# Optimization experiments

Hardware: AMD Instinct MI355X
Metric: run time of the kernel (lower is better)

The kernel has to match this reference:

```python
import jax, jax.numpy as jnp
import numpy as np

N, C, T, V = 16, 256, 400, 27
S, CI, O = 2, 64, 256      # num_subset, inter_channels, out_channels
OFFSET = 2                  # LearnedPositionalEmbedding offset
EPS = 1e-5                  # BatchNorm eps (inference/eval mode)


def _bn(x, g, b, m, v):
    # BatchNorm2d in eval mode: (x - mean)/sqrt(var+eps)*gamma + beta, per-channel
    return (x - m[None, :, None, None]) / jnp.sqrt(v[None, :, None, None] + EPS) \
        * g[None, :, None, None] + b[None, :, None, None]


def setup_inputs() -> dict:
    key = jax.random.key(0)
    ks = jax.random.split(key, 24)
    u = lambda k, s: jax.random.uniform(k, s, jnp.float32, 0.5, 1.5)
    r = lambda k, s, sc: jax.random.normal(k, s, jnp.float32) * sc
    d = {}
    d['x'] = jax.random.normal(ks[0], (N, C, T, V), jnp.float32)
    # learned positional embedding table: (num_frame + offset, num_node)
    d['pe'] = r(ks[1], (400 + OFFSET, V), 0.02)
    # in_nets: 1x1 conv C -> 2*S*CI
    d['in_w'] = r(ks[2], (2 * S * CI, C), 0.02)
    d['in_b'] = jnp.zeros((2 * S * CI,), jnp.float32)
    d['alphas'] = jnp.ones((1, S, 1, 1), jnp.float32)
    d['att0'] = jnp.ones((1, S, V, V), jnp.float32) / V   # attention0s
    # out_nets: 1x1 conv S*C -> O, then BN1
    d['out_w'] = r(ks[3], (O, S * C), 0.02)
    d['out_b'] = jnp.zeros((O,), jnp.float32)
    d['bn1_g'] = u(ks[4], (O,)); d['bn1_b'] = r(ks[5], (O,), 0.1)
    d['bn1_m'] = r(ks[6], (O,), 0.1); d['bn1_v'] = u(ks[7], (O,))
    # ff_nets: 1x1 conv O -> O, then BN2
    d['ff_w'] = r(ks[8], (O, O), 0.02)
    d['ff_b'] = jnp.zeros((O,), jnp.float32)
    d['bn2_g'] = u(ks[9], (O,)); d['bn2_b'] = r(ks[10], (O,), 0.1)
    d['bn2_m'] = r(ks[11], (O,), 0.1); d['bn2_v'] = u(ks[12], (O,))
    # out_nett: (3,1) temporal conv O -> O, then BN3
    d['t_w'] = r(ks[13], (O, O, 3, 1), 0.02)
    d['t_b'] = jnp.zeros((O,), jnp.float32)
    d['bn3_g'] = u(ks[14], (O,)); d['bn3_b'] = r(ks[15], (O,), 0.1)
    d['bn3_m'] = r(ks[16], (O,), 0.1); d['bn3_v'] = u(ks[17], (O,))
    return d


def reference(x, pe, in_w, in_b, alphas, att0, out_w, out_b,
              bn1_g, bn1_b, bn1_m, bn1_v, ff_w, ff_b,
              bn2_g, bn2_b, bn2_m, bn2_v, t_w, t_b,
              bn3_g, bn3_b, bn3_m, bn3_v):
    n, c, t, v = x.shape
    # learned positional embedding over frame index (shared across batch*channel)
    pos = pe[jnp.arange(t) + OFFSET]              # (T, V)
    y = x + pos[None, None, :, :]                 # (N, C, T, V)
    # in_nets 1x1 conv -> q, k
    qk = jnp.einsum('nctv,oc->notv', y, in_w) + in_b[None, :, None, None]
    qk = qk.reshape(n, 2 * S, CI, t, v)
    q, k = qk[:, :S], qk[:, S:]                   # (N, S, CI, T, V) each
    attn = jnp.einsum('nsctu,nsctv->nsuv', q, k) / (CI * t) * alphas + att0
    attn = jax.nn.softmax(attn, axis=-1)          # (N, S, V, V)  (dropout p=0)
    # re-aggregate values with original x
    y2 = jnp.einsum('nctu,nsuv->nsctv', x, attn).reshape(n, S * c, t, v)
    y2 = jnp.einsum('nctv,oc->notv', y2, out_w) + out_b[None, :, None, None]
    y2 = _bn(y2, bn1_g, bn1_b, bn1_m, bn1_v)
    y1 = jax.nn.leaky_relu(x + y2, 0.1)           # downs1 = identity (C==O)
    y2 = jnp.einsum('nctv,oc->notv', y1, ff_w) + ff_b[None, :, None, None]
    y2 = _bn(y2, bn2_g, bn2_b, bn2_m, bn2_v)
    y1 = jax.nn.leaky_relu(x + y2, 0.1)           # downs2 = identity
    # temporal branch (use_temporal_att=False): (3,1) conv + BN + residual
    z = jax.lax.conv_general_dilated(
        y1, t_w, window_strides=(1, 1), padding=((1, 1), (0, 0)),
        dimension_numbers=('NCHW', 'OIHW', 'NCHW')) + t_b[None, :, None, None]
    z = _bn(z, bn3_g, bn3_b, bn3_m, bn3_v)
    return jax.nn.leaky_relu(y1 + z, 0.1)         # downt2 = identity
```

## Files before the change

### kernel.cpp

```cpp
#include <hip/hip_runtime.h>
#include <hip/hip_bf16.h>
#include <cstddef>

#define NBATCH 16
#define CCH    256
#define TT     400
#define VV     27
#define TV     10800
#define EPSV   1e-5f
#define P2     10854

typedef __attribute__((ext_vector_type(8))) short  short8;
typedef __attribute__((ext_vector_type(4))) float  floatx4;

__device__ __forceinline__ unsigned short f2bu(float f) {
    __hip_bfloat16 h = __float2bfloat16(f);
    return *(unsigned short*)&h;
}
__device__ __forceinline__ float bu2f(unsigned short u) {
    union { float f; unsigned int i; } c; c.i = ((unsigned int)u) << 16; return c.f;
}
__device__ __forceinline__ void gl_lds16(const void* g, void* l) {
    __builtin_amdgcn_global_load_lds(
        (const __attribute__((address_space(1))) void*)g,
        (__attribute__((address_space(3))) void*)l, 16, 0, 0);
}

template<int KC, int MODE>
__global__ __launch_bounds__(512) void mfma_gemm(
    const unsigned short* __restrict__ X8,
    const unsigned short* __restrict__ W8,
    const float* __restrict__ bias,
    const float* __restrict__ bng, const float* __restrict__ bnb,
    const float* __restrict__ bnm, const float* __restrict__ bnv,
    const unsigned short* __restrict__ res8,
    const float* __restrict__ pe,
    float* __restrict__ outf,
    unsigned short* __restrict__ out8)
{
    constexpr int XPITCH = (MODE == 3) ? P2 : TV;
    constexpr int XOFF   = (MODE == 3) ? 27 : 0;
    constexpr int XROWS  = (MODE == 3) ? 32 : (KC / 8);
    constexpr int OPITCH = (MODE == 2) ? P2 : TV;
    constexpr int OOFF   = (MODE == 2) ? 27 : 0;
    constexpr int NSTEP  = KC / 32;

    __shared__ short Ws[3][4096];
    __shared__ short Xs[3][8192];
    __shared__ float scs[128], shs[128];

    const int tid  = threadIdx.x;
    const int wid  = tid >> 6;
    const int lane = tid & 63;
    const int quad = lane >> 4, col = lane & 15;

    const int bid = blockIdx.x;
    const int g   = bid >> 4;
    const int r   = bid & 15;
    const int oy  = r >> 3;
    const int j   = g * 8 + (r & 7);
    const int px  = j % 43;
    const int n   = j / 43;
    const int p0 = px * 256;
    const int o0 = oy * 128;

    const int wo = (wid >> 2) * 64;
    const int wp = (wid & 3) * 64;

    const size_t nX = (size_t)n * XROWS * XPITCH;

    auto stage = [&](int buf, int step) {
        int k0, c0, pshift = 0;
        if constexpr (MODE == 3) {
            const int ccs = step / 3;
            const int kt  = step - ccs * 3;
            k0 = kt * 256 + ccs * 32;
            c0 = ccs * 32;
            pshift = 27 * (kt - 1);
        } else {
            k0 = step * 32;
            c0 = k0;
        }
        #pragma unroll
        for (int q = 0; q < 3; q++) {
            const int ci = wid * 3 + q;
            if (ci < 8) {
                const int kg = ci >> 1, half = ci & 1;
                const size_t woff = ((size_t)((k0 >> 3) + kg) * 256 + o0 + half * 64 + lane) * 8;
                gl_lds16(W8 + woff, &Ws[buf][ci * 512]);
            } else {
                const int xi = ci - 8;
                const int kg = xi >> 2, q4 = xi & 3;
                const size_t xoff = (nX + (size_t)((c0 >> 3) + kg) * XPITCH
                                     + XOFF + p0 + pshift + q4 * 64 + lane) * 8;
                gl_lds16(X8 + xoff, &Xs[buf][xi * 512]);
            }
        }
    };

    floatx4 acc[4][4];
    #pragma unroll
    for (int i = 0; i < 4; i++)
        #pragma unroll
        for (int j2 = 0; j2 < 4; j2++)
            acc[i][j2] = (floatx4){0.f, 0.f, 0.f, 0.f};

    stage(0, 0);
    stage(1, 1);

    int cur = 0;
    for (int step = 0; step < NSTEP; ++step) {
        if (step + 1 < NSTEP) asm volatile("s_waitcnt vmcnt(3)" ::: "memory");
        else                  asm volatile("s_waitcnt vmcnt(0)" ::: "memory");
        __builtin_amdgcn_s_barrier();
        if (step + 2 < NSTEP) stage((cur + 2 >= 3) ? cur - 1 : cur + 2, step + 2);
        short8 a[4], b[4];
        #pragma unroll
        for (int i = 0; i < 4; i++)
            a[i] = *(const short8*)&Ws[cur][quad * 1024 + (wo + i * 16 + col) * 8];
        #pragma unroll
        for (int j2 = 0; j2 < 4; j2++)
            b[j2] = *(const short8*)&Xs[cur][quad * 2048 + (wp + j2 * 16 + col) * 8];
        __builtin_amdgcn_s_setprio(1);
        #pragma unroll
        for (int i = 0; i < 4; i++)
            #pragma unroll
            for (int j2 = 0; j2 < 4; j2++)
                acc[i][j2] = __builtin_amdgcn_mfma_f32_16x16x32_bf16(a[i], b[j2], acc[i][j2], 0, 0, 0);
        __builtin_amdgcn_s_setprio(0);
        cur = (cur == 2) ? 0 : cur + 1;
    }

    __syncthreads();

    if (tid < 128) {
        const int o = o0 + tid;
        float sc, sh;
        if constexpr (MODE == 0) { sc = 1.f; sh = bias[o]; }
        else {
            const float g2 = bng[o], b2 = bnb[o], m = bnm[o], v2 = bnv[o];
            sc = g2 * rsqrtf(v2 + EPSV);
            sh = bias[o] * sc + b2 - m * sc;
        }
        scs[tid] = sc; shs[tid] = sh;
    }
    __syncthreads();

    #pragma unroll
    for (int i = 0; i < 4; i++) {
        const int ol = wo + i * 16 + quad * 4;
        const int ob = o0 + ol;
        #pragma unroll
        for (int j2 = 0; j2 < 4; j2++) {
            const int p = p0 + wp + j2 * 16 + col;
            if (p >= TV) continue;
            float v[4];
            #pragma unroll
            for (int r2 = 0; r2 < 4; r2++)
                v[r2] = acc[i][j2][r2] * scs[ol + r2] + shs[ol + r2];
            if constexpr (MODE == 3) {
                const size_t roff = ((size_t)n * 32 * P2 + (size_t)(ob >> 3) * P2 + 27 + p) * 8 + (ob & 7);
                union { unsigned long long u64; unsigned short us[4]; } rr;
                rr.u64 = *(const unsigned long long*)&res8[roff];
                #pragma unroll
                for (int r2 = 0; r2 < 4; r2++) {
                    float t = v[r2] + bu2f(rr.us[r2]);
                    t = t > 0.f ? t : 0.1f * t;
                    outf[((size_t)n * 256 + ob + r2) * TV + p] = t;
                }
            } else if constexpr (MODE == 0) {
                union { unsigned long long u64; unsigned short us[4]; } pk;
                #pragma unroll
                for (int r2 = 0; r2 < 4; r2++) pk.us[r2] = f2bu(v[r2]);
                *(unsigned long long*)&out8[((size_t)n * 32 * TV
                    + (size_t)(ob >> 3) * TV + p) * 8 + (ob & 7)] = pk.u64;
            } else {
                const float pev = pe[p + 54];
                const size_t roff = ((size_t)n * 32 * TV + (size_t)(ob >> 3) * TV + p) * 8 + (ob & 7);
                union { unsigned long long u64; unsigned short us[4]; } rr;
                rr.u64 = *(const unsigned long long*)&res8[roff];
                union { unsigned long long u64; unsigned short us[4]; } pk;
                #pragma unroll
                for (int r2 = 0; r2 < 4; r2++) {
                    float t = v[r2] + (bu2f(rr.us[r2]) - pev);
                    t = t > 0.f ? t : 0.1f * t;
                    pk.us[r2] = f2bu(t);
                }
                *(unsigned long long*)&out8[((size_t)n * 32 * OPITCH
                    + (size_t)(ob >> 3) * OPITCH + OOFF + p) * 8 + (ob & 7)] = pk.u64;
            }
        }
    }
}

__global__ __launch_bounds__(256) void prep_xpe(
    const float* __restrict__ x, const float* __restrict__ pe,
    unsigned short* __restrict__ xpe8)
{
    const int p = blockIdx.x * 256 + threadIdx.x;
    const int cg = blockIdx.y, n = blockIdx.z;
    if (p >= TV) return;
    const float pev = pe[p + 54];
    const float* xp = x + ((size_t)n * 256 + cg * 8) * TV + p;
    union { unsigned short us[8]; uint4 q; } pk;
    #pragma unroll
    for (int r = 0; r < 8; r++)
        pk.us[r] = f2bu(xp[(size_t)r * TV] + pev);
    *(uint4*)&xpe8[(((size_t)n * 32 + cg) * TV + p) * 8] = pk.q;
}

__global__ void pack_w(const float* __restrict__ w, unsigned short* __restrict__ w8,
                       int KCc, int conv)
{
    const int idx = blockIdx.x * 256 + threadIdx.x;
    if (idx >= 256 * KCc) return;
    const int o = idx / KCc, k = idx - o * KCc;
    float v;
    if (conv) { const int c = k & 255, kt = k >> 8; v = w[((size_t)o * 256 + c) * 3 + kt]; }
    else v = w[(size_t)o * KCc + k];
    w8[((size_t)(k >> 3) * 256 + o) * 8 + (k & 7)] = f2bu(v);
}

__global__ void zero_pads(unsigned short* __restrict__ y1b8) {
    unsigned short* base = y1b8 + (size_t)blockIdx.x * P2 * 8;
    for (int i = threadIdx.x; i < 27 * 8; i += 256) {
        base[i] = 0;
        base[10827 * 8 + i] = 0;
    }
}

__global__ __launch_bounds__(256) void attn_logits_mfma(
    const unsigned short* __restrict__ qk8, float* __restrict__ logits)
{
    __shared__ float red[4][32][33];
    const int tid  = threadIdx.x;
    const int wid  = tid >> 6;
    const int lane = tid & 63;
    const int quad = lane >> 4, col = lane & 15;
    const int tch = blockIdx.x;
    const int ns  = blockIdx.y;
    const int n = ns >> 1, s = ns & 1;
    const int t0 = tch * 16 + wid * 4;

    const unsigned short* qb = qk8 + (size_t)(n * 32 + s * 8) * TV * 8;
    const unsigned short* kb = qk8 + (size_t)(n * 32 + 16 + s * 8) * TV * 8;

    floatx4 acc[2][2];
    #pragma unroll
    for (int i = 0; i < 2; i++)
        #pragma unroll
        for (int j = 0; j < 2; j++)
            acc[i][j] = (floatx4){0.f, 0.f, 0.f, 0.f};

    #pragma unroll
    for (int ti = 0; ti < 4; ti++) {
        const int t = t0 + ti;
        #pragma unroll
        for (int kk = 0; kk < 2; kk++) {
            const size_t ro = ((size_t)(kk * 4 + quad) * TV + t * 27 + col) * 8;
            const short8 a0 = *(const short8*)&qb[ro];
            const short8 a1 = *(const short8*)&qb[ro + 128];
            const short8 b0 = *(const short8*)&kb[ro];
            const short8 b1 = *(const short8*)&kb[ro + 128];
            acc[0][0] = __builtin_amdgcn_mfma_f32_16x16x32_bf16(a0, b0, acc[0][0], 0, 0, 0);
            acc[0][1] = __builtin_amdgcn_mfma_f32_16x16x32_bf16(a0, b1, acc[0][1], 0, 0, 0);
            acc[1][0] = __builtin_amdgcn_mfma_f32_16x16x32_bf16(a1, b0, acc[1][0], 0, 0, 0);
            acc[1][1] = __builtin_amdgcn_mfma_f32_16x16x32_bf16(a1, b1, acc[1][1], 0, 0, 0);
        }
    }

    #pragma unroll
    for (int i = 0; i < 2; i++)
        #pragma unroll
        for (int j = 0; j < 2; j++)
            #pragma unroll
            for (int r = 0; r < 4; r++)
                red[wid][i * 16 + quad * 4 + r][j * 16 + col] = acc[i][j][r];
    __syncthreads();
    for (int e = tid; e < 729; e += 256) {
        const int u = e / 27, v = e - u * 27;
        atomicAdd(&logits[(size_t)ns * 729 + e],
                  red[0][u][v] + red[1][u][v] + red[2][u][v] + red[3][u][v]);
    }
}

__global__ __launch_bounds__(64) void attn_softmax(
    const float* __restrict__ logits, const float* __restrict__ alphas,
    const float* __restrict__ att0, float* __restrict__ attn)
{
    const int ns = blockIdx.x;
    const int s = ns & 1;
    const int u = threadIdx.x;
    if (u < 27) {
        float row[27];
        const float alpha = alphas[s];
        const float inv_ct = 1.f / 25600.f;
        float m = -1e30f;
        for (int v = 0; v < 27; v++) {
            const float val = logits[(size_t)ns * 729 + u * 27 + v] * inv_ct * alpha
                            + att0[(size_t)(s * 27 + u) * 27 + v];
            row[v] = val;
            m = fmaxf(m, val);
        }
        float sum = 0.f;
        for (int v = 0; v < 27; v++) { row[v] = __expf(row[v] - m); sum += row[v]; }
        const float inv = 1.f / sum;
        for (int v = 0; v < 27; v++)
            attn[(size_t)ns * 729 + u * 27 + v] = row[v] * inv;
    }
}

__global__ __launch_bounds__(256) void xa_mfma(
    const float* __restrict__ x, const float* __restrict__ attn,
    unsigned short* __restrict__ xa8)
{
    __shared__ unsigned short xs[16][16][40];
    const int tid  = threadIdx.x;
    const int wid  = tid >> 6;
    const int lane = tid & 63;
    const int quad = lane >> 4, col = lane & 15;
    const int tch = blockIdx.x;
    const int c0  = blockIdx.y * 16;
    const int n   = blockIdx.z;

    short8 bf[2][2];
    #pragma unroll
    for (int s = 0; s < 2; s++) {
        const float* ab = attn + (size_t)(n * 2 + s) * 729;
        #pragma unroll
        for (int vt = 0; vt < 2; vt++) {
            const int v = vt * 16 + col;
            #pragma unroll
            for (int e = 0; e < 8; e++) {
                const int u = quad * 8 + e;
                bf[s][vt][e] = (u < 27 && v < 27) ? (short)f2bu(ab[u * 27 + v]) : (short)0;
            }
        }
    }

    for (int idx = tid; idx < 16 * 16 * 5; idx += 256) {
        const int t = idx / 80;
        const int r = idx - t * 80;
        const int c = r / 5;
        xs[t][c][27 + (r - c * 5)] = 0;
    }

    const float* xbase = x + ((size_t)n * 256 + c0) * TV + tch * 432;
    for (int idx = tid; idx < 16 * 108; idx += 256) {
        const int row = idx / 108;
        const int q   = idx - row * 108;
        const int j   = q * 4;
        int t = (j * 607) >> 14;
        int u = j - t * 27;
        const float4 f = *(const float4*)&xbase[(size_t)row * TV + j];
        float e4[4] = {f.x, f.y, f.z, f.w};
        #pragma unroll
        for (int r = 0; r < 4; r++) {
            xs[t][row][u] = f2bu(e4[r]);
            if (++u == 27) { u = 0; ++t; }
        }
    }
    __syncthreads();

    #pragma unroll
    for (int ti = 0; ti < 4; ti++) {
        const int tl = wid * 4 + ti;
        const int t  = tch * 16 + tl;
        const short8 af = *(const short8*)&xs[tl][col][quad * 8];
        #pragma unroll
        for (int s = 0; s < 2; s++) {
            #pragma unroll
            for (int vt = 0; vt < 2; vt++) {
                floatx4 d = __builtin_amdgcn_mfma_f32_16x16x32_bf16(
                    af, bf[s][vt], (floatx4){0.f, 0.f, 0.f, 0.f}, 0, 0, 0);
                const int v = vt * 16 + col;
                if (v < 27) {
                    const size_t cgg = (size_t)n * 64 + s * 32 + (c0 >> 3) + (quad >> 1);
                    union { unsigned long long u64; unsigned short us[4]; } pk;
                    #pragma unroll
                    for (int r = 0; r < 4; r++) pk.us[r] = f2bu(d[r]);
                    *(unsigned long long*)&xa8[(cgg * TV + t * 27 + v) * 8 + (quad & 1) * 4] = pk.u64;
                }
            }
        }
    }
}

extern "C" void kernel_launch(void* const* d_in, const int* in_sizes, int n_in,
                              void* d_out, int out_size, void* d_ws, size_t ws_size,
                              hipStream_t stream) {
    const float* x      = (const float*)d_in[0];
    const float* pe     = (const float*)d_in[1];
    const float* in_w   = (const float*)d_in[2];
    const float* in_b   = (const float*)d_in[3];
    const float* alphas = (const float*)d_in[4];
    const float* att0   = (const float*)d_in[5];
    const float* out_w  = (const float*)d_in[6];
    const float* out_b  = (const float*)d_in[7];
    const float* bn1_g  = (const float*)d_in[8];
    const float* bn1_b  = (const float*)d_in[9];
    const float* bn1_m  = (const float*)d_in[10];
    const float* bn1_v  = (const float*)d_in[11];
    const float* ff_w   = (const float*)d_in[12];
    const float* ff_b   = (const float*)d_in[13];
    const float* bn2_g  = (const float*)d_in[14];
    const float* bn2_b  = (const float*)d_in[15];
    const float* bn2_m  = (const float*)d_in[16];
    const float* bn2_v  = (const float*)d_in[17];
    const float* t_w    = (const float*)d_in[18];
    const float* t_b    = (const float*)d_in[19];
    const float* bn3_g  = (const float*)d_in[20];
    const float* bn3_b  = (const float*)d_in[21];
    const float* bn3_m  = (const float*)d_in[22];
    const float* bn3_v  = (const float*)d_in[23];

    char* ws = (char*)d_ws;
    const size_t A_BYTES = (size_t)16 * 32 * TV * 8 * 2 + 8192;
    const size_t B_BYTES = (size_t)16 * 256 * TV * 4 + 8192;
    const size_t C_BYTES = (size_t)16 * 32 * P2 * 8 * 2 + 8192;
    unsigned short* xpe8 = (unsigned short*)ws;
    unsigned short* qk8  = (unsigned short*)(ws + A_BYTES);
    unsigned short* xa8  = (unsigned short*)(ws + A_BYTES);
    unsigned short* y1b8 = (unsigned short*)(ws + A_BYTES);
    unsigned short* y1_8 = (unsigned short*)(ws + A_BYTES + B_BYTES);
    char* D = ws + A_BYTES + B_BYTES + C_BYTES;
    float* logits = (float*)D;
    float* attn   = (float*)(D + 93440);
    unsigned short* w1_8 = (unsigned short*)(D + 2 * 93440);
    unsigned short* w4_8 = w1_8 + (size_t)256 * 256;
    unsigned short* w5_8 = w4_8 + (size_t)256 * 512;
    unsigned short* w6_8 = w5_8 + (size_t)256 * 256;

    pack_w<<<256, 256, 0, stream>>>(in_w,  w1_8, 256, 0);
    pack_w<<<512, 256, 0, stream>>>(out_w, w4_8, 512, 0);
    pack_w<<<256, 256, 0, stream>>>(ff_w,  w5_8, 256, 0);
    pack_w<<<768, 256, 0, stream>>>(t_w,   w6_8, 768, 1);
    prep_xpe<<<dim3(43, 32, 16), 256, 0, stream>>>(x, pe, xpe8);

    const int NWG = 1376;

    mfma_gemm<256, 0><<<NWG, 512, 0, stream>>>(
        xpe8, w1_8, in_b, nullptr, nullptr, nullptr, nullptr, nullptr, nullptr, nullptr, qk8);

    hipMemsetAsync(logits, 0, (size_t)NBATCH * 2 * 729 * sizeof(float), stream);
    attn_logits_mfma<<<dim3(25, NBATCH * 2), 256, 0, stream>>>(qk8, logits);
    attn_softmax<<<NBATCH * 2, 64, 0, stream>>>(logits, alphas, att0, attn);

    xa_mfma<<<dim3(25, 16, 16), 256, 0, stream>>>(x, attn, xa8);

    mfma_gemm<512, 1><<<NWG, 512, 0, stream>>>(
        xa8, w4_8, out_b, bn1_g, bn1_b, bn1_m, bn1_v, xpe8, pe, nullptr, y1_8);

    zero_pads<<<512, 256, 0, stream>>>(y1b8);

    mfma_gemm<256, 2><<<NWG, 512, 0, stream>>>(
        y1_8, w5_8, ff_b, bn2_g, bn2_b, bn2_m, bn2_v, xpe8, pe, nullptr, y1b8);

    mfma_gemm<768, 3><<<NWG, 512, 0, stream>>>(
        y1b8, w6_8, t_b, bn3_g, bn3_b, bn3_m, bn3_v, y1b8, nullptr, (float*)d_out, nullptr);
}
```

Before: 808.2 us.

## Enlarge GEMM tile to all 256 output channels with double-buffered K=64 steps

Each workgroup of the pointwise GEMM kernel now computes all 256 output channels for a 256-position tile instead of 128, halving the grid and removing the duplicate load of the activation tile across the two output halves. The K loop moves from triple-buffered 32-wide steps to double-buffered 64-wide steps, with two barriers per step. Per-wave accumulators double to 8x4 MFMA tiles, which raises register pressure and LDS use (64KB) and lowers occupancy. The grid shrinks to 688 workgroups, which may leave compute units less evenly loaded.

Measured after the change: 847.8 us. 1.05x slower.

```diff
diff --git a/kernel.cpp b/kernel.cpp
--- a/kernel.cpp
+++ b/kernel.cpp
@@ -43,11 +43,11 @@
     constexpr int XROWS  = (MODE == 3) ? 32 : (KC / 8);
     constexpr int OPITCH = (MODE == 2) ? P2 : TV;
     constexpr int OOFF   = (MODE == 2) ? 27 : 0;
-    constexpr int NSTEP  = KC / 32;
-
-    __shared__ short Ws[3][4096];
-    __shared__ short Xs[3][8192];
-    __shared__ float scs[128], shs[128];
+    constexpr int NK     = KC / 64;
+
+    __shared__ short Ws[2][16384];
+    __shared__ short Xs[2][16384];
+    __shared__ float scs[256], shs[256];
 
     const int tid  = threadIdx.x;
     const int wid  = tid >> 6;
@@ -55,86 +55,83 @@
     const int quad = lane >> 4, col = lane & 15;
 
     const int bid = blockIdx.x;
-    const int g   = bid >> 4;
-    const int r   = bid & 15;
-    const int oy  = r >> 3;
-    const int j   = g * 8 + (r & 7);
-    const int px  = j % 43;
-    const int n   = j / 43;
-    const int p0 = px * 256;
-    const int o0 = oy * 128;
-
-    const int wo = (wid >> 2) * 64;
+    const int px  = bid % 43;
+    const int n   = bid / 43;
+    const int p0  = px * 256;
+
+    const int wo = (wid >> 2) * 128;
     const int wp = (wid & 3) * 64;
 
     const size_t nX = (size_t)n * XROWS * XPITCH;
 
-    auto stage = [&](int buf, int step) {
+    auto stage = [&](int buf, int t) {
         int k0, c0, pshift = 0;
         if constexpr (MODE == 3) {
-            const int ccs = step / 3;
-            const int kt  = step - ccs * 3;
-            k0 = kt * 256 + ccs * 32;
-            c0 = ccs * 32;
-            pshift = 27 * (kt - 1);
+            const int ccs = t / 3;
+            const int tap = t - ccs * 3;
+            k0 = tap * 256 + ccs * 64;
+            c0 = ccs * 64;
+            pshift = 27 * (tap - 1);
         } else {
-            k0 = step * 32;
+            k0 = t * 64;
             c0 = k0;
         }
         #pragma unroll
-        for (int q = 0; q < 3; q++) {
-            const int ci = wid * 3 + q;
-            if (ci < 8) {
-                const int kg = ci >> 1, half = ci & 1;
-                const size_t woff = ((size_t)((k0 >> 3) + kg) * 256 + o0 + half * 64 + lane) * 8;
-                gl_lds16(W8 + woff, &Ws[buf][ci * 512]);
-            } else {
-                const int xi = ci - 8;
-                const int kg = xi >> 2, q4 = xi & 3;
-                const size_t xoff = (nX + (size_t)((c0 >> 3) + kg) * XPITCH
-                                     + XOFF + p0 + pshift + q4 * 64 + lane) * 8;
-                gl_lds16(X8 + xoff, &Xs[buf][xi * 512]);
-            }
+        for (int q = 0; q < 4; q++) {
+            const size_t woff = ((size_t)((k0 >> 3) + wid) * 256 + q * 64 + lane) * 8;
+            gl_lds16(W8 + woff, &Ws[buf][((size_t)wid * 256 + q * 64 + lane) * 8]);
+        }
+        #pragma unroll
+        for (int q = 0; q < 4; q++) {
+            const size_t xoff = (nX + (size_t)((c0 >> 3) + wid) * XPITCH
+                                 + XOFF + p0 + pshift + q * 64 + lane) * 8;
+            gl_lds16(X8 + xoff, &Xs[buf][((size_t)wid * 256 + q * 64 + lane) * 8]);
         }
     };
 
-    floatx4 acc[4][4];
-    #pragma unroll
-    for (int i = 0; i < 4; i++)
+    floatx4 acc[8][4];
+    #pragma unroll
+    for (int i = 0; i < 8; i++)
         #pragma unroll
         for (int j2 = 0; j2 < 4; j2++)
             acc[i][j2] = (floatx4){0.f, 0.f, 0.f, 0.f};
 
     stage(0, 0);
-    stage(1, 1);
-
-    int cur = 0;
-    for (int step = 0; step < NSTEP; ++step) {
-        if (step + 1 < NSTEP) asm volatile("s_waitcnt vmcnt(3)" ::: "memory");
-        else                  asm volatile("s_waitcnt vmcnt(0)" ::: "memory");
+
+    for (int kt = 0; kt < NK; ++kt) {
+        const int cur = kt & 1;
         __builtin_amdgcn_s_barrier();
-        if (step + 2 < NSTEP) stage((cur + 2 >= 3) ? cur - 1 : cur + 2, step + 2);
-        short8 a[4], b[4];
-        #pragma unroll
-        for (int i = 0; i < 4; i++)
-            a[i] = *(const short8*)&Ws[cur][quad * 1024 + (wo + i * 16 + col) * 8];
-        #pragma unroll
-        for (int j2 = 0; j2 < 4; j2++)
-            b[j2] = *(const short8*)&Xs[cur][quad * 2048 + (wp + j2 * 16 + col) * 8];
-        __builtin_amdgcn_s_setprio(1);
-        #pragma unroll
-        for (int i = 0; i < 4; i++)
+        if (kt + 1 < NK) {
+            stage(cur ^ 1, kt + 1);
+            asm volatile("s_waitcnt vmcnt(8)" ::: "memory");
+        } else {
+            asm volatile("s_waitcnt vmcnt(0)" ::: "memory");
+        }
+        __builtin_amdgcn_s_barrier();
+
+        #pragma unroll
+        for (int kh = 0; kh < 2; ++kh) {
+            const int kg = kh * 4 + quad;
+            short8 b[4];
             #pragma unroll
             for (int j2 = 0; j2 < 4; j2++)
-                acc[i][j2] = __builtin_amdgcn_mfma_f32_16x16x32_bf16(a[i], b[j2], acc[i][j2], 0, 0, 0);
-        __builtin_amdgcn_s_setprio(0);
-        cur = (cur == 2) ? 0 : cur + 1;
+                b[j2] = *(const short8*)&Xs[cur][((size_t)kg * 256 + wp + j2 * 16 + col) * 8];
+            __builtin_amdgcn_s_setprio(1);
+            #pragma unroll
+            for (int i = 0; i < 8; i++) {
+                const short8 a = *(const short8*)&Ws[cur][((size_t)kg * 256 + wo + i * 16 + col) * 8];
+                #pragma unroll
+                for (int j2 = 0; j2 < 4; j2++)
+                    acc[i][j2] = __builtin_amdgcn_mfma_f32_16x16x32_bf16(a, b[j2], acc[i][j2], 0, 0, 0);
+            }
+            __builtin_amdgcn_s_setprio(0);
+        }
     }
 
     __syncthreads();
 
-    if (tid < 128) {
-        const int o = o0 + tid;
+    if (tid < 256) {
+        const int o = tid;
         float sc, sh;
         if constexpr (MODE == 0) { sc = 1.f; sh = bias[o]; }
         else {
@@ -147,9 +144,8 @@
     __syncthreads();
 
     #pragma unroll
-    for (int i = 0; i < 4; i++) {
-        const int ol = wo + i * 16 + quad * 4;
-        const int ob = o0 + ol;
+    for (int i = 0; i < 8; i++) {
+        const int ob = wo + i * 16 + quad * 4;
         #pragma unroll
         for (int j2 = 0; j2 < 4; j2++) {
             const int p = p0 + wp + j2 * 16 + col;
@@ -157,7 +153,7 @@
             float v[4];
             #pragma unroll
             for (int r2 = 0; r2 < 4; r2++)
-                v[r2] = acc[i][j2][r2] * scs[ol + r2] + shs[ol + r2];
+                v[r2] = acc[i][j2][r2] * scs[ob + r2] + shs[ob + r2];
             if constexpr (MODE == 3) {
                 const size_t roff = ((size_t)n * 32 * P2 + (size_t)(ob >> 3) * P2 + 27 + p) * 8 + (ob & 7);
                 union { unsigned long long u64; unsigned short us[4]; } rr;
@@ -437,7 +433,7 @@
     pack_w<<<768, 256, 0, stream>>>(t_w,   w6_8, 768, 1);
     prep_xpe<<<dim3(43, 32, 16), 256, 0, stream>>>(x, pe, xpe8);
 
-    const int NWG = 1376;
+    const int NWG = 43 * 16;
 
     mfma_gemm<256, 0><<<NWG, 512, 0, stream>>>(
         xpe8, w1_8, in_b, nullptr, nullptr, nullptr, nullptr, nullptr, nullptr, nullptr, qk8);
```
